# Kernel optimization log

Hardware: AMD Instinct MI355X
Metric: run time of the kernel (lower is better)

## Reference

```python
import jax, jax.numpy as jnp
import numpy as np

B, D_IN, D_OUT, E = 8192, 1024, 1024, 16


def setup_inputs() -> dict:
    key = jax.random.key(0)
    k1, k2, k3 = jax.random.split(key, 3)
    x = jax.random.normal(k1, (B, D_IN), dtype=jnp.float32)
    Wg = jax.random.normal(k2, (D_IN, E), dtype=jnp.float32) * (1.0 / np.sqrt(D_IN))
    bg = jnp.zeros((E,), dtype=jnp.float32)
    We = jax.random.normal(k3, (E, D_IN, D_OUT), dtype=jnp.float32) * (1.0 / np.sqrt(D_IN))
    be = jnp.zeros((E, D_OUT), dtype=jnp.float32)
    return {"x": x, "Wg": Wg, "bg": bg, "We": We, "be": be}


def reference(x, Wg, bg, We, be):
    # Gate: [B, E]
    gate_out = x @ Wg + bg
    top1 = jnp.argmax(gate_out, axis=1)  # [B]
    # All-expert dense compute (faithful to the naive HardMoE): [B, E, D_OUT]
    expert_outs = jnp.einsum('bd,edh->beh', x, We) + be[None, :, :]
    # Gather each row's argmax expert output: [B, D_OUT]
    out = jnp.take_along_axis(expert_outs, top1[:, None, None], axis=1)[:, 0, :]
    return out
```

## Files before the change

kernel.cpp:

```cpp
#include <hip/hip_runtime.h>

typedef unsigned short u16;
typedef __attribute__((ext_vector_type(4))) unsigned short u16x4;
typedef __attribute__((ext_vector_type(8))) short short8;
typedef __attribute__((ext_vector_type(4))) float floatx4;

#define NB 8192
#define DK 1024
#define DN 1024
#define NE 16
#define TM 128
#define TN 128
#define BK 64
#define MAX_TILES 80

__device__ __forceinline__ u16 f2bf(float f) {
    union { float f; unsigned int u; } v; v.f = f;
    unsigned int u = v.u;
    return (u16)((u + 0x7fffu + ((u >> 16) & 1u)) >> 16);
}

__device__ __forceinline__ void gld16(const void* g, void* l) {
    __builtin_amdgcn_global_load_lds(
        (const __attribute__((address_space(1))) unsigned int*)g,
        (__attribute__((address_space(3))) unsigned int*)l, 16, 0, 0);
}

__global__ void k_init(int* cnt) {
    if (threadIdx.x < NE) cnt[threadIdx.x] = 0;
}

__global__ __launch_bounds__(256) void k_gate(const float* __restrict__ x,
                                              const float* __restrict__ Wg,
                                              const float* __restrict__ bg,
                                              u16* __restrict__ xb,
                                              int* __restrict__ cnt,
                                              int* __restrict__ bucket) {
    __shared__ float xs[16 * 132];
    __shared__ float wgs[16 * 132];
    const int tid = threadIdx.x;
    const int R0 = blockIdx.x * 16;
    const int row_l = tid >> 4;
    const int e = tid & 15;

    double a0 = (double)bg[e], a1 = 0.0, a2 = 0.0, a3 = 0.0;

    for (int ci = 0; ci < 8; ++ci) {
        const int i0 = ci * 128;
        #pragma unroll
        for (int h = 0; h < 2; ++h) {
            int f = h * 256 + tid;
            int r = f >> 5;
            int i4 = (f & 31) * 4;
            float4 v = *(const float4*)&x[(size_t)(R0 + r) * DK + i0 + i4];
            *(float4*)&xs[r * 132 + i4] = v;
            u16x4 b; b.x = f2bf(v.x); b.y = f2bf(v.y); b.z = f2bf(v.z); b.w = f2bf(v.w);
            *(u16x4*)&xb[(size_t)(R0 + r) * DK + i0 + i4] = b;
        }
        #pragma unroll
        for (int h = 0; h < 2; ++h) {
            int g = h * 256 + tid;
            int i = g >> 2;
            int e4 = (g & 3) * 4;
            float4 v = *(const float4*)&Wg[(size_t)(i0 + i) * NE + e4];
            wgs[(e4 + 0) * 132 + i] = v.x;
            wgs[(e4 + 1) * 132 + i] = v.y;
            wgs[(e4 + 2) * 132 + i] = v.z;
            wgs[(e4 + 3) * 132 + i] = v.w;
        }
        __syncthreads();
        #pragma unroll 8
        for (int i4 = 0; i4 < 32; ++i4) {
            float4 xv = *(const float4*)&xs[row_l * 132 + i4 * 4];
            float4 wv = *(const float4*)&wgs[e * 132 + i4 * 4];
            a0 += (double)xv.x * (double)wv.x;
            a1 += (double)xv.y * (double)wv.y;
            a2 += (double)xv.z * (double)wv.z;
            a3 += (double)xv.w * (double)wv.w;
        }
        __syncthreads();
    }
    double acc = (a0 + a1) + (a2 + a3);

    double best = acc; int bi = e;
    #pragma unroll
    for (int off = 8; off >= 1; off >>= 1) {
        double ov = __shfl_xor(best, off);
        int    oi = __shfl_xor(bi, off);
        if (ov > best || (ov == best && oi < bi)) { best = ov; bi = oi; }
    }
    if (e == 0) {
        int pos = atomicAdd(&cnt[bi], 1);
        bucket[bi * NB + pos] = R0 + row_l;
    }
}

__global__ __launch_bounds__(256) void k_wet(const float* __restrict__ We,
                                             u16* __restrict__ WeT) {
    __shared__ u16 t[64 * 68];
    const int e = blockIdx.z;
    const int n0 = blockIdx.y * 64;
    const int k0 = blockIdx.x * 64;
    const int tid = threadIdx.x;
    const float* src = We + (size_t)e * DK * DN;
    const int kl = tid >> 4;
    const int n4 = (tid & 15) * 4;
    #pragma unroll
    for (int r = 0; r < 4; ++r) {
        int k = kl + r * 16;
        float4 v = *(const float4*)&src[(size_t)(k0 + k) * DN + n0 + n4];
        t[(n4 + 0) * 68 + k] = f2bf(v.x);
        t[(n4 + 1) * 68 + k] = f2bf(v.y);
        t[(n4 + 2) * 68 + k] = f2bf(v.z);
        t[(n4 + 3) * 68 + k] = f2bf(v.w);
    }
    __syncthreads();
    u16* dst = WeT + (size_t)e * DN * DK;
    #pragma unroll
    for (int r = 0; r < 4; ++r) {
        int c = r * 256 + tid;
        int nl = c >> 4;
        int kq = (c & 15) * 4;
        *(u16x4*)&dst[(size_t)(n0 + nl) * DK + k0 + kq] = *(const u16x4*)&t[nl * 68 + kq];
    }
}

__global__ void k_tiles(const int* __restrict__ cnt, int* __restrict__ list,
                        int* __restrict__ total) {
    if (threadIdx.x == 0) {
        int t = 0;
        for (int e = 0; e < NE; ++e) {
            int n = (cnt[e] + TM - 1) / TM;
            for (int i = 0; i < n; ++i) list[t++] = (e << 16) | i;
        }
        *total = t;
    }
}

__global__ __launch_bounds__(256) void k_moe(const u16* __restrict__ xb,
                                             const u16* __restrict__ WeT,
                                             const float* __restrict__ be,
                                             const int* __restrict__ bucket,
                                             const int* __restrict__ cnt,
                                             const int* __restrict__ list,
                                             const int* __restrict__ total,
                                             float* __restrict__ out) {
    const int slot = blockIdx.x >> 3;
    const int nt = blockIdx.x & 7;
    if (slot >= *total) return;
    const int ent = list[slot];
    const int e = ent >> 16;
    const int mt = ent & 0xffff;
    const int cntE = cnt[e];
    const int m0 = mt * TM;
    const int n0 = nt * TN;

    __shared__ u16 aLds[TM * BK];
    __shared__ u16 bLds[TN * BK];

    const int tid = threadIdx.x;
    const int lane = tid & 63;
    const int w = tid >> 6;
    const int wr = w >> 1, wc = w & 1;
    const int lr = lane & 15, q = lane >> 4;

    long aoff[4]; long boff[4]; int ldsb[4];
    #pragma unroll
    for (int r = 0; r < 4; ++r) {
        int c = r * 256 + tid;
        int row = c >> 3;
        int k8 = (c & 7) ^ (row & 7);
        int m_idx = m0 + row; if (m_idx >= cntE) m_idx = cntE - 1;
        long rid = bucket[e * NB + m_idx];
        aoff[r] = rid * DK + k8 * 8;
        boff[r] = (long)e * DN * DK + (long)(n0 + row) * DK + k8 * 8;
        ldsb[r] = (r * 256 + (tid & ~63)) * 8;
    }

    floatx4 acc[4][4];
    #pragma unroll
    for (int mi = 0; mi < 4; ++mi)
        #pragma unroll
        for (int ni = 0; ni < 4; ++ni)
            acc[mi][ni] = (floatx4)0.0f;

    for (int kk = 0; kk < DK; kk += BK) {
        #pragma unroll
        for (int r = 0; r < 4; ++r) {
            gld16(xb + aoff[r] + kk, &aLds[ldsb[r]]);
            gld16(WeT + boff[r] + kk, &bLds[ldsb[r]]);
        }
        __syncthreads();
        #pragma unroll
        for (int ks = 0; ks < 2; ++ks) {
            short8 af[4], bfr[4];
            const int slot_k = ((ks << 2) + q) ^ (lr & 7);
            #pragma unroll
            for (int mi = 0; mi < 4; ++mi) {
                int row = wr * 64 + mi * 16 + lr;
                af[mi] = *(const short8*)&aLds[row * BK + slot_k * 8];
                int nrow = wc * 64 + mi * 16 + lr;
                bfr[mi] = *(const short8*)&bLds[nrow * BK + slot_k * 8];
            }
            #pragma unroll
            for (int mi = 0; mi < 4; ++mi)
                #pragma unroll
                for (int ni = 0; ni < 4; ++ni)
                    acc[mi][ni] = __builtin_amdgcn_mfma_f32_16x16x32_bf16(
                        af[mi], bfr[ni], acc[mi][ni], 0, 0, 0);
        }
        __syncthreads();
    }

    float bias[4];
    #pragma unroll
    for (int ni = 0; ni < 4; ++ni)
        bias[ni] = be[e * DN + n0 + wc * 64 + ni * 16 + lr];

    #pragma unroll
    for (int mi = 0; mi < 4; ++mi) {
        #pragma unroll
        for (int rr = 0; rr < 4; ++rr) {
            int row_l = wr * 64 + mi * 16 + q * 4 + rr;
            int m_idx = m0 + row_l;
            if (m_idx < cntE) {
                long rid = bucket[e * NB + m_idx];
                float* orow = out + rid * DN + n0 + wc * 64 + lr;
                #pragma unroll
                for (int ni = 0; ni < 4; ++ni)
                    orow[ni * 16] = acc[mi][ni][rr] + bias[ni];
            }
        }
    }
}

extern "C" void kernel_launch(void* const* d_in, const int* in_sizes, int n_in,
                              void* d_out, int out_size, void* d_ws, size_t ws_size,
                              hipStream_t stream) {
    const float* x  = (const float*)d_in[0];
    const float* Wg = (const float*)d_in[1];
    const float* bg = (const float*)d_in[2];
    const float* We = (const float*)d_in[3];
    const float* be = (const float*)d_in[4];
    float* out = (float*)d_out;

    int* cnt    = (int*)d_ws;
    int* total  = cnt + 16;
    int* tlist  = cnt + 32;
    int* bucket = cnt + 128;
    u16* xb  = (u16*)((char*)d_ws + (1u << 20));
    u16* wet = (u16*)((char*)d_ws + (18u << 20));

    k_init<<<1, 64, 0, stream>>>(cnt);
    k_gate<<<NB / 16, 256, 0, stream>>>(x, Wg, bg, xb, cnt, bucket);
    k_wet<<<dim3(16, 16, 16), 256, 0, stream>>>(We, wet);
    k_tiles<<<1, 64, 0, stream>>>(cnt, tlist, total);
    k_moe<<<MAX_TILES * 8, 256, 0, stream>>>(xb, wet, be, bucket, cnt, tlist, total, out);
}
```

Before: 233.7 us.

## Merge gate and weight-transpose kernels, compute tile list inside MoE kernel

Combines the gate/argmax kernel and the expert weight bf16 transpose into one launch, with the block index choosing which role each block takes. The gate part now does register tiling (4 rows by 4 experts per thread, with a shuffle reduction over k). The separate tile-list kernel goes away: each MoE block derives its expert and m-tile from the counts, and the init kernel becomes a memset. This removes several launches and their serialization and lets gate and transpose work overlap, at the cost of extra per-block count scanning and a changed double-precision accumulation order in the gate.

```diff
diff --git a/kernel.cpp b/kernel.cpp
--- a/kernel.cpp
+++ b/kernel.cpp
@@ -14,6 +14,9 @@
 #define BK 64
 #define MAX_TILES 80
 
+#define GATE_BLOCKS 256
+#define WET_BLOCKS  4096
+
 __device__ __forceinline__ u16 f2bf(float f) {
     union { float f; unsigned int u; } v; v.f = f;
     unsigned int u = v.u;
@@ -26,114 +29,138 @@
         (__attribute__((address_space(3))) unsigned int*)l, 16, 0, 0);
 }
 
-__global__ void k_init(int* cnt) {
-    if (threadIdx.x < NE) cnt[threadIdx.x] = 0;
-}
-
-__global__ __launch_bounds__(256) void k_gate(const float* __restrict__ x,
+__global__ __launch_bounds__(256) void k_prep(const float* __restrict__ x,
                                               const float* __restrict__ Wg,
                                               const float* __restrict__ bg,
+                                              const float* __restrict__ We,
                                               u16* __restrict__ xb,
+                                              u16* __restrict__ WeT,
                                               int* __restrict__ cnt,
                                               int* __restrict__ bucket) {
-    __shared__ float xs[16 * 132];
-    __shared__ float wgs[16 * 132];
+    __shared__ union {
+        struct { float xs[32 * 132]; float wgs[16 * 132]; } g;
+        u16 t[64 * 68];
+    } sh;
+
     const int tid = threadIdx.x;
-    const int R0 = blockIdx.x * 16;
-    const int row_l = tid >> 4;
-    const int e = tid & 15;
-
-    double a0 = (double)bg[e], a1 = 0.0, a2 = 0.0, a3 = 0.0;
-
-    for (int ci = 0; ci < 8; ++ci) {
-        const int i0 = ci * 128;
-        #pragma unroll
-        for (int h = 0; h < 2; ++h) {
-            int f = h * 256 + tid;
-            int r = f >> 5;
-            int i4 = (f & 31) * 4;
-            float4 v = *(const float4*)&x[(size_t)(R0 + r) * DK + i0 + i4];
-            *(float4*)&xs[r * 132 + i4] = v;
-            u16x4 b; b.x = f2bf(v.x); b.y = f2bf(v.y); b.z = f2bf(v.z); b.w = f2bf(v.w);
-            *(u16x4*)&xb[(size_t)(R0 + r) * DK + i0 + i4] = b;
-        }
-        #pragma unroll
-        for (int h = 0; h < 2; ++h) {
-            int g = h * 256 + tid;
-            int i = g >> 2;
-            int e4 = (g & 3) * 4;
-            float4 v = *(const float4*)&Wg[(size_t)(i0 + i) * NE + e4];
-            wgs[(e4 + 0) * 132 + i] = v.x;
-            wgs[(e4 + 1) * 132 + i] = v.y;
-            wgs[(e4 + 2) * 132 + i] = v.z;
-            wgs[(e4 + 3) * 132 + i] = v.w;
+
+    if (blockIdx.x < GATE_BLOCKS) {
+        const int kg = tid & 7;
+        const int eg = (tid >> 3) & 3;
+        const int rg = tid >> 5;
+        const int R0 = blockIdx.x * 32;
+
+        float* xs  = sh.g.xs;
+        float* wgs = sh.g.wgs;
+
+        double acc[4][4];
+        #pragma unroll
+        for (int i = 0; i < 4; ++i)
+            #pragma unroll
+            for (int j = 0; j < 4; ++j) acc[i][j] = 0.0;
+
+        for (int c = 0; c < 8; ++c) {
+            const int k0 = c * 128;
+            #pragma unroll
+            for (int it = 0; it < 4; ++it) {
+                int f = it * 256 + tid;
+                int r = f >> 5;
+                int k4 = (f & 31) * 4;
+                float4 v = *(const float4*)&x[(size_t)(R0 + r) * DK + k0 + k4];
+                *(float4*)&xs[r * 132 + k4] = v;
+                u16x4 b; b.x = f2bf(v.x); b.y = f2bf(v.y); b.z = f2bf(v.z); b.w = f2bf(v.w);
+                *(u16x4*)&xb[(size_t)(R0 + r) * DK + k0 + k4] = b;
+            }
+            #pragma unroll
+            for (int it = 0; it < 2; ++it) {
+                int g = it * 256 + tid;
+                int k = g >> 2;
+                int e4 = (g & 3) * 4;
+                float4 v = *(const float4*)&Wg[(size_t)(k0 + k) * NE + e4];
+                wgs[(e4 + 0) * 132 + k] = v.x;
+                wgs[(e4 + 1) * 132 + k] = v.y;
+                wgs[(e4 + 2) * 132 + k] = v.z;
+                wgs[(e4 + 3) * 132 + k] = v.w;
+            }
+            __syncthreads();
+            #pragma unroll
+            for (int t = 0; t < 4; ++t) {
+                const int ko = t * 32 + kg * 4;
+                float4 xq[4], wq[4];
+                #pragma unroll
+                for (int i = 0; i < 4; ++i)
+                    xq[i] = *(const float4*)&xs[(rg * 4 + i) * 132 + ko];
+                #pragma unroll
+                for (int j = 0; j < 4; ++j)
+                    wq[j] = *(const float4*)&wgs[(eg * 4 + j) * 132 + ko];
+                #pragma unroll
+                for (int i = 0; i < 4; ++i)
+                    #pragma unroll
+                    for (int j = 0; j < 4; ++j) {
+                        acc[i][j] += (double)xq[i].x * (double)wq[j].x;
+                        acc[i][j] += (double)xq[i].y * (double)wq[j].y;
+                        acc[i][j] += (double)xq[i].z * (double)wq[j].z;
+                        acc[i][j] += (double)xq[i].w * (double)wq[j].w;
+                    }
+            }
+            __syncthreads();
+        }
+
+        #pragma unroll
+        for (int i = 0; i < 4; ++i)
+            #pragma unroll
+            for (int j = 0; j < 4; ++j) {
+                double v = acc[i][j];
+                v += __shfl_xor(v, 1);
+                v += __shfl_xor(v, 2);
+                v += __shfl_xor(v, 4);
+                acc[i][j] = v + (double)bg[eg * 4 + j];
+            }
+
+        #pragma unroll
+        for (int i = 0; i < 4; ++i) {
+            double best = acc[i][0]; int bi = eg * 4;
+            #pragma unroll
+            for (int j = 1; j < 4; ++j)
+                if (acc[i][j] > best) { best = acc[i][j]; bi = eg * 4 + j; }
+            #pragma unroll
+            for (int off = 8; off <= 16; off <<= 1) {
+                double ov = __shfl_xor(best, off);
+                int    oi = __shfl_xor(bi, off);
+                if (ov > best || (ov == best && oi < bi)) { best = ov; bi = oi; }
+            }
+            if (kg == 0 && eg == 0) {
+                int pos = atomicAdd(&cnt[bi], 1);
+                bucket[bi * NB + pos] = R0 + rg * 4 + i;
+            }
+        }
+    } else {
+        const int bw = blockIdx.x - GATE_BLOCKS;
+        const int e  = bw >> 8;
+        const int n0 = ((bw >> 4) & 15) * 64;
+        const int k0 = (bw & 15) * 64;
+        u16* t = sh.t;
+        const float* src = We + (size_t)e * DK * DN;
+        const int kl = tid >> 4;
+        const int n4 = (tid & 15) * 4;
+        #pragma unroll
+        for (int r = 0; r < 4; ++r) {
+            int k = kl + r * 16;
+            float4 v = *(const float4*)&src[(size_t)(k0 + k) * DN + n0 + n4];
+            t[(n4 + 0) * 68 + k] = f2bf(v.x);
+            t[(n4 + 1) * 68 + k] = f2bf(v.y);
+            t[(n4 + 2) * 68 + k] = f2bf(v.z);
+            t[(n4 + 3) * 68 + k] = f2bf(v.w);
         }
         __syncthreads();
-        #pragma unroll 8
-        for (int i4 = 0; i4 < 32; ++i4) {
-            float4 xv = *(const float4*)&xs[row_l * 132 + i4 * 4];
-            float4 wv = *(const float4*)&wgs[e * 132 + i4 * 4];
-            a0 += (double)xv.x * (double)wv.x;
-            a1 += (double)xv.y * (double)wv.y;
-            a2 += (double)xv.z * (double)wv.z;
-            a3 += (double)xv.w * (double)wv.w;
-        }
-        __syncthreads();
-    }
-    double acc = (a0 + a1) + (a2 + a3);
-
-    double best = acc; int bi = e;
-    #pragma unroll
-    for (int off = 8; off >= 1; off >>= 1) {
-        double ov = __shfl_xor(best, off);
-        int    oi = __shfl_xor(bi, off);
-        if (ov > best || (ov == best && oi < bi)) { best = ov; bi = oi; }
-    }
-    if (e == 0) {
-        int pos = atomicAdd(&cnt[bi], 1);
-        bucket[bi * NB + pos] = R0 + row_l;
-    }
-}
-
-__global__ __launch_bounds__(256) void k_wet(const float* __restrict__ We,
-                                             u16* __restrict__ WeT) {
-    __shared__ u16 t[64 * 68];
-    const int e = blockIdx.z;
-    const int n0 = blockIdx.y * 64;
-    const int k0 = blockIdx.x * 64;
-    const int tid = threadIdx.x;
-    const float* src = We + (size_t)e * DK * DN;
-    const int kl = tid >> 4;
-    const int n4 = (tid & 15) * 4;
-    #pragma unroll
-    for (int r = 0; r < 4; ++r) {
-        int k = kl + r * 16;
-        float4 v = *(const float4*)&src[(size_t)(k0 + k) * DN + n0 + n4];
-        t[(n4 + 0) * 68 + k] = f2bf(v.x);
-        t[(n4 + 1) * 68 + k] = f2bf(v.y);
-        t[(n4 + 2) * 68 + k] = f2bf(v.z);
-        t[(n4 + 3) * 68 + k] = f2bf(v.w);
-    }
-    __syncthreads();
-    u16* dst = WeT + (size_t)e * DN * DK;
-    #pragma unroll
-    for (int r = 0; r < 4; ++r) {
-        int c = r * 256 + tid;
-        int nl = c >> 4;
-        int kq = (c & 15) * 4;
-        *(u16x4*)&dst[(size_t)(n0 + nl) * DK + k0 + kq] = *(const u16x4*)&t[nl * 68 + kq];
-    }
-}
-
-__global__ void k_tiles(const int* __restrict__ cnt, int* __restrict__ list,
-                        int* __restrict__ total) {
-    if (threadIdx.x == 0) {
-        int t = 0;
-        for (int e = 0; e < NE; ++e) {
-            int n = (cnt[e] + TM - 1) / TM;
-            for (int i = 0; i < n; ++i) list[t++] = (e << 16) | i;
-        }
-        *total = t;
+        u16* dst = WeT + (size_t)e * DN * DK;
+        #pragma unroll
+        for (int r = 0; r < 4; ++r) {
+            int c = r * 256 + tid;
+            int nl = c >> 4;
+            int kq = (c & 15) * 4;
+            *(u16x4*)&dst[(size_t)(n0 + nl) * DK + k0 + kq] = *(const u16x4*)&t[nl * 68 + kq];
+        }
     }
 }
 
@@ -142,16 +169,20 @@
                                              const float* __restrict__ be,
                                              const int* __restrict__ bucket,
                                              const int* __restrict__ cnt,
-                                             const int* __restrict__ list,
-                                             const int* __restrict__ total,
                                              float* __restrict__ out) {
     const int slot = blockIdx.x >> 3;
     const int nt = blockIdx.x & 7;
-    if (slot >= *total) return;
-    const int ent = list[slot];
-    const int e = ent >> 16;
-    const int mt = ent & 0xffff;
-    const int cntE = cnt[e];
+
+    int e = -1, mt = 0, cntE = 0, acc_t = 0;
+    #pragma unroll
+    for (int ee = 0; ee < NE; ++ee) {
+        int ce = cnt[ee];
+        int nte = (ce + TM - 1) / TM;
+        if (e < 0 && slot < acc_t + nte) { e = ee; mt = slot - acc_t; cntE = ce; }
+        acc_t += nte;
+    }
+    if (e < 0) return;
+
     const int m0 = mt * TM;
     const int n0 = nt * TN;
 
@@ -245,15 +276,11 @@
     float* out = (float*)d_out;
 
     int* cnt    = (int*)d_ws;
-    int* total  = cnt + 16;
-    int* tlist  = cnt + 32;
     int* bucket = cnt + 128;
     u16* xb  = (u16*)((char*)d_ws + (1u << 20));
     u16* wet = (u16*)((char*)d_ws + (18u << 20));
 
-    k_init<<<1, 64, 0, stream>>>(cnt);
-    k_gate<<<NB / 16, 256, 0, stream>>>(x, Wg, bg, xb, cnt, bucket);
-    k_wet<<<dim3(16, 16, 16), 256, 0, stream>>>(We, wet);
-    k_tiles<<<1, 64, 0, stream>>>(cnt, tlist, total);
-    k_moe<<<MAX_TILES * 8, 256, 0, stream>>>(xb, wet, be, bucket, cnt, tlist, total, out);
-}
+    hipMemsetAsync(cnt, 0, 16 * sizeof(int), stream);
+    k_prep<<<GATE_BLOCKS + WET_BLOCKS, 256, 0, stream>>>(x, Wg, bg, We, xb, wet, cnt, bucket);
+    k_moe<<<MAX_TILES * 8, 256, 0, stream>>>(xb, wet, be, bucket, cnt, out);
+}
```

Result: slower. 239.4 us (+2.4%).
